# Performance work log

Measured on AMD Instinct MI355X. Metric: run time of the kernel, lower is better.

Reference implementation:

```python
import jax, jax.numpy as jnp
import numpy as np

B, T, D, H = 4, 2048, 1024, 16
HS = D // H  # 64
SCALE = float(HS) ** (-5)  # faithful to source: head_size ** (-5), NOT -0.5
EPS = 1e-5


def layer_norm(x, g, b):
    m = jnp.mean(x, axis=-1, keepdims=True)
    v = jnp.mean(jnp.square(x - m), axis=-1, keepdims=True)
    return (x - m) * jax.lax.rsqrt(v + EPS) * g + b


def setup_inputs() -> dict:
    key = jax.random.key(0)
    ks = jax.random.split(key, 8)
    s = 0.02
    return {
        "x": jax.random.normal(ks[0], (B, T, D), dtype=jnp.float32),
        "Wk": jax.random.normal(ks[1], (H, D, HS), dtype=jnp.float32) * s,  # shared by q (source bug: q = self.key(x))
        "Wv": jax.random.normal(ks[2], (H, D, HS), dtype=jnp.float32) * s,
        "Wo": jax.random.normal(ks[3], (H * HS, D), dtype=jnp.float32) * s,
        "bo": jnp.zeros((D,), dtype=jnp.float32),
        "g1": jnp.ones((D,), dtype=jnp.float32),
        "b1": jnp.zeros((D,), dtype=jnp.float32),
        "Wf1": jax.random.normal(ks[4], (D, D), dtype=jnp.float32) * s,
        "bf1": jnp.zeros((D,), dtype=jnp.float32),
        "Wf2": jax.random.normal(ks[5], (D, D), dtype=jnp.float32) * s,
        "bf2": jnp.zeros((D,), dtype=jnp.float32),
        "g2": jnp.ones((D,), dtype=jnp.float32),
        "b2": jnp.zeros((D,), dtype=jnp.float32),
    }


def reference(x, Wk, Wv, Wo, bo, g1, b1, Wf1, bf1, Wf2, bf2, g2, b2):
    # per-head projections; source uses key weights for BOTH q and k, so q == k
    k = jnp.einsum('btd,hds->bhts', x, Wk)           # [B,H,T,HS]
    v = jnp.einsum('btd,hds->bhts', x, Wv)           # [B,H,T,HS]
    wei = jnp.einsum('bhts,bhus->bhtu', k, k) * SCALE  # q==k; [B,H,T,T]
    causal = jnp.tril(jnp.ones((T, T), dtype=bool))
    wei = jnp.where(causal, wei, -jnp.inf)
    wei = jax.nn.softmax(wei, axis=-1)
    attn = jnp.einsum('bhtu,bhus->bhts', wei, v)     # [B,H,T,HS]
    cat = attn.transpose(0, 2, 1, 3).reshape(B, T, H * HS)  # concat heads
    attn_out = cat @ Wo + bo                         # output projection
    norm = layer_norm(attn_out + x, g1, b1)
    ff = jax.nn.relu(norm @ Wf1 + bf1) @ Wf2 + bf2
    return layer_norm(ff + norm + x, g2, b2)
```

## Files before the change

kernel.cpp:

```cpp
#include <hip/hip_runtime.h>

typedef unsigned short u16;
typedef __attribute__((ext_vector_type(8))) short short8;
typedef __attribute__((ext_vector_type(4))) float f32x4;

constexpr int Bn = 4, Tn = 2048, Dn = 1024, Hn = 16, HSn = 64;
constexpr long BT = (long)Bn * Tn;
#define NSEG 64
#define SEG (Tn / NSEG)

__device__ __forceinline__ u16 f2bf(float f) {
    union { float f; unsigned u; } x; x.f = f;
    unsigned r = x.u + 0x7FFFu + ((x.u >> 16) & 1u);
    return (u16)(r >> 16);
}
__device__ __forceinline__ float bf2f(unsigned bits16) {
    union { unsigned u; float f; } x; x.u = bits16 << 16;
    return x.f;
}

__device__ __forceinline__ void async_load16(const u16* g, u16* lds) {
    __builtin_amdgcn_global_load_lds(
        (const __attribute__((address_space(1))) unsigned*)g,
        (__attribute__((address_space(3))) unsigned*)lds, 16, 0, 0);
}

__global__ __launch_bounds__(256) void prep_kernel(
    const float* __restrict__ x, const float* __restrict__ Wv,
    const float* __restrict__ Wo, const float* __restrict__ Wf1,
    const float* __restrict__ Wf2,
    u16* __restrict__ xb, u16* __restrict__ WvC,
    u16* __restrict__ WoT, u16* __restrict__ Wf1T, u16* __restrict__ Wf2T)
{
    __shared__ float tile[32][33];
    const int blk = blockIdx.x;
    if (blk < 8192) {
        long i = (long)blk * 256 + threadIdx.x;
        float4 v = ((const float4*)x)[i];
        unsigned lo = (unsigned)f2bf(v.x) | ((unsigned)f2bf(v.y) << 16);
        unsigned hi = (unsigned)f2bf(v.z) | ((unsigned)f2bf(v.w) << 16);
        ((uint2*)xb)[i] = make_uint2(lo, hi);
    } else if (blk < 12288) {
        long i = (long)(blk - 8192) * 256 + threadIdx.x;
        int d = (int)(i >> 10), c = (int)(i & 1023);
        int h = c >> 6, s = c & 63;
        WvC[i] = f2bf(Wv[((long)h * Dn + d) * HSn + s]);
    } else {
        int idx = blk - 12288;
        int z = idx >> 10, rem = idx & 1023;
        const float* in = z == 0 ? Wo : (z == 1 ? Wf1 : Wf2);
        u16* out        = z == 0 ? WoT : (z == 1 ? Wf1T : Wf2T);
        int k0 = (rem & 31) * 32, n0 = (rem >> 5) * 32;
        int tx = threadIdx.x & 31, ty = threadIdx.x >> 5;
        #pragma unroll
        for (int r = 0; r < 4; r++)
            tile[ty + r * 8][tx] = in[(long)(k0 + ty + r * 8) * Dn + n0 + tx];
        __syncthreads();
        #pragma unroll
        for (int r = 0; r < 4; r++)
            out[(long)(n0 + ty + r * 8) * Dn + k0 + tx] = f2bf(tile[tx][ty + r * 8]);
    }
}

__device__ __forceinline__ void stageA256(const u16* __restrict__ Ag, u16* la,
                                          int r, int wv, int ln, int row0,
                                          int K, int kt) {
    int Ib = r * 512 + wv * 64;
    int I = Ib + ln;
    int m = I >> 3, pc = I & 7, c = pc ^ (m & 7);
    async_load16(&Ag[(long)(row0 + m) * K + kt * 64 + c * 8], &la[Ib * 8]);
}
__device__ __forceinline__ void stageB256(const u16* __restrict__ Bg, u16* lb,
                                          int r, int wv, int ln, int n0,
                                          int K, int kt) {
    int Ib = r * 512 + wv * 64;
    int I = Ib + ln;
    int m = I >> 3, pc = I & 7, c = pc ^ (m & 7);
    async_load16(&Bg[(long)(n0 + m) * K + kt * 64 + c * 8], &lb[Ib * 8]);
}
__device__ __forceinline__ short8 ldfrag(const u16* ls, int row, int lc) {
    return *(const short8*)&ls[(row * 8 + (lc ^ (row & 7))) * 8];
}

__global__ __launch_bounds__(512) void mfma_gemm256(
    const u16* __restrict__ A,
    const u16* __restrict__ BTm,
    u16* __restrict__ Cb,
    const float* __restrict__ bias, int relu, int K, int N,
    float* __restrict__ segs_out)
{
    __shared__ __attribute__((aligned(16))) u16 As[3][256 * 64];
    __shared__ __attribute__((aligned(16))) u16 Bs[3][128 * 64];

    const int t = threadIdx.x;
    const int wv = t >> 6, ln = t & 63;
    const int lane15 = ln & 15, qq = ln >> 4;
    const int wr = wv >> 2, wc = wv & 3;
    const int row0 = blockIdx.x * 256, n0 = blockIdx.y * 128;
    const int NT = K >> 6;

    f32x4 acc[8][2];
    #pragma unroll
    for (int i = 0; i < 8; i++)
        #pragma unroll
        for (int j = 0; j < 2; j++)
            acc[i][j] = (f32x4){0.f, 0.f, 0.f, 0.f};

    u16 *A0 = &As[0][0], *A1 = &As[1][0], *A2 = &As[2][0];
    u16 *B0 = &Bs[0][0], *B1 = &Bs[1][0], *B2 = &Bs[2][0];

    #pragma unroll
    for (int r = 0; r < 4; r++) stageA256(A, A0, r, wv, ln, row0, K, 0);
    #pragma unroll
    for (int r = 0; r < 2; r++) stageB256(BTm, B0, r, wv, ln, n0, K, 0);
    #pragma unroll
    for (int r = 0; r < 4; r++) stageA256(A, A1, r, wv, ln, row0, K, 1);
    #pragma unroll
    for (int r = 0; r < 2; r++) stageB256(BTm, B1, r, wv, ln, n0, K, 1);
    asm volatile("s_waitcnt vmcnt(6)" ::: "memory");
    __builtin_amdgcn_s_barrier();

    for (int kt = 0; kt < NT; kt++) {
        const bool st = (kt + 2 < NT);
        short8 bq[2][2];
        #pragma unroll
        for (int ph = 0; ph < 4; ph++) {
            short8 af[2][2];
            #pragma unroll
            for (int ii = 0; ii < 2; ii++) {
                int ar = wr * 128 + (ph * 2 + ii) * 16 + lane15;
                af[ii][0] = ldfrag(A0, ar, qq);
                af[ii][1] = ldfrag(A0, ar, 4 + qq);
            }
            if (ph == 0) {
                #pragma unroll
                for (int ng = 0; ng < 2; ng++) {
                    int br = wc * 32 + ng * 16 + lane15;
                    bq[ng][0] = ldfrag(B0, br, qq);
                    bq[ng][1] = ldfrag(B0, br, 4 + qq);
                }
                if (st) {
                    stageA256(A, A2, 0, wv, ln, row0, K, kt + 2);
                    stageA256(A, A2, 1, wv, ln, row0, K, kt + 2);
                }
            } else if (ph == 1) {
                if (st) {
                    stageA256(A, A2, 2, wv, ln, row0, K, kt + 2);
                    stageA256(A, A2, 3, wv, ln, row0, K, kt + 2);
                }
            } else if (ph == 2) {
                if (st) {
                    stageB256(BTm, B2, 0, wv, ln, n0, K, kt + 2);
                    stageB256(BTm, B2, 1, wv, ln, n0, K, kt + 2);
                }
            }
            __builtin_amdgcn_s_barrier();
            __builtin_amdgcn_s_setprio(1);
            #pragma unroll
            for (int kk = 0; kk < 2; kk++)
                #pragma unroll
                for (int ii = 0; ii < 2; ii++)
                    #pragma unroll
                    for (int ng = 0; ng < 2; ng++)
                        acc[ph * 2 + ii][ng] = __builtin_amdgcn_mfma_f32_16x16x32_bf16(
                            af[ii][kk], bq[ng][kk], acc[ph * 2 + ii][ng], 0, 0, 0);
            __builtin_amdgcn_s_setprio(0);
            if (ph < 3) {
                __builtin_amdgcn_s_barrier();
            } else if (kt < NT - 1) {
                if (st) asm volatile("s_waitcnt vmcnt(6)" ::: "memory");
                else    asm volatile("s_waitcnt vmcnt(0)" ::: "memory");
                __builtin_amdgcn_s_barrier();
            }
        }
        u16* ta = A0; A0 = A1; A1 = A2; A2 = ta;
        u16* tb = B0; B0 = B1; B1 = B2; B2 = tb;
    }

    if (segs_out) {
        int segbase = blockIdx.x * 8 + wr * 4;
        #pragma unroll
        for (int s = 0; s < 4; s++) {
            #pragma unroll
            for (int ng = 0; ng < 2; ng++) {
                float sum = 0.f;
                #pragma unroll
                for (int r = 0; r < 4; r++)
                    sum += acc[2 * s][ng][r] + acc[2 * s + 1][ng][r];
                sum += __shfl_xor(sum, 16);
                sum += __shfl_xor(sum, 32);
                if (qq == 0) {
                    int col = n0 + wc * 32 + ng * 16 + lane15;
                    segs_out[(long)(segbase + s) * N + col] = sum;
                }
            }
        }
    }

    #pragma unroll
    for (int ng = 0; ng < 2; ng++) {
        int col = n0 + wc * 32 + ng * 16 + lane15;
        float bv = bias ? bias[col] : 0.f;
        #pragma unroll
        for (int i = 0; i < 8; i++) {
            #pragma unroll
            for (int r = 0; r < 4; r++) {
                long row = row0 + wr * 128 + i * 16 + qq * 4 + r;
                float v = acc[i][ng][r] + bv;
                if (relu) v = fmaxf(v, 0.f);
                Cb[row * N + col] = f2bf(v);
            }
        }
    }
}

__global__ __launch_bounds__(256) void mfma_gemm64(
    const u16* __restrict__ A, const u16* __restrict__ BT,
    u16* __restrict__ Cb, int K, int N)
{
    __shared__ __attribute__((aligned(16))) u16 As[64 * 64];
    __shared__ __attribute__((aligned(16))) u16 Bs[64 * 64];

    const int t = threadIdx.x;
    const int wv = t >> 6, ln = t & 63;
    const int lane15 = ln & 15, q = ln >> 4;
    const int row0 = blockIdx.x * 64, n0 = blockIdx.y * 64;
    const int mq = (wv >> 1) * 32, nq = (wv & 1) * 32;

    f32x4 acc[2][2];
    #pragma unroll
    for (int i = 0; i < 2; i++)
        #pragma unroll
        for (int j = 0; j < 2; j++)
            acc[i][j] = (f32x4){0.f, 0.f, 0.f, 0.f};

    for (int k0 = 0; k0 < K; k0 += 64) {
        #pragma unroll
        for (int jj = 0; jj < 2; jj++) {
            int Ibase = wv * 128 + jj * 64;
            int I = Ibase + ln;
            int m = I >> 3, pc = I & 7, c = pc ^ (m & 7);
            async_load16(&A[(long)(row0 + m) * K + k0 + c * 8], &As[Ibase * 8]);
        }
        #pragma unroll
        for (int jj = 0; jj < 2; jj++) {
            int Ibase = wv * 128 + jj * 64;
            int I = Ibase + ln;
            int m = I >> 3, pc = I & 7, c = pc ^ (m & 7);
            async_load16(&BT[(long)(n0 + m) * K + k0 + c * 8], &Bs[Ibase * 8]);
        }
        __syncthreads();

        #pragma unroll
        for (int kk = 0; kk < 2; kk++) {
            short8 af[2], bfr[2];
            #pragma unroll
            for (int i = 0; i < 2; i++) {
                int mr = mq + i * 16 + lane15;
                int ca = (kk * 4 + q) ^ (mr & 7);
                af[i] = *(const short8*)&As[(mr * 8 + ca) * 8];
                int nr = nq + i * 16 + lane15;
                int cb = (kk * 4 + q) ^ (nr & 7);
                bfr[i] = *(const short8*)&Bs[(nr * 8 + cb) * 8];
            }
            #pragma unroll
            for (int i = 0; i < 2; i++)
                #pragma unroll
                for (int j = 0; j < 2; j++)
                    acc[i][j] = __builtin_amdgcn_mfma_f32_16x16x32_bf16(
                        af[i], bfr[j], acc[i][j], 0, 0, 0);
        }
        __syncthreads();
    }

    #pragma unroll
    for (int j = 0; j < 2; j++) {
        int col = n0 + nq + j * 16 + lane15;
        #pragma unroll
        for (int i = 0; i < 2; i++)
            #pragma unroll
            for (int r = 0; r < 4; r++) {
                long row = row0 + mq + i * 16 + q * 4 + r;
                Cb[row * N + col] = f2bf(acc[i][j][r]);
            }
    }
}

__global__ __launch_bounds__(256) void scanln_kernel(
    const u16* __restrict__ y, const float* __restrict__ segs,
    const float* __restrict__ bo, const u16* __restrict__ xb,
    const float* __restrict__ g1, const float* __restrict__ b1,
    u16* __restrict__ nb)
{
    __shared__ float zs[16 * 1024];

    const int b = blockIdx.x, sg = blockIdx.y;
    const int t = threadIdx.x;
    const int lane = t & 63, w = t >> 6;

    float r0 = 0.f, r1 = 0.f, r2 = 0.f, r3 = 0.f;
    for (int s = 0; s < sg; s++) {
        float4 sv = ((const float4*)&segs[((long)(b * NSEG + s)) * Dn])[t];
        r0 += sv.x; r1 += sv.y; r2 += sv.z; r3 += sv.w;
    }
    const float4 bv = ((const float4*)bo)[t];

    float gv[16], be[16];
    #pragma unroll
    for (int j = 0; j < 4; j++) {
        *(float4*)&gv[j * 4] = *(const float4*)(g1 + j * 256 + lane * 4);
        *(float4*)&be[j * 4] = *(const float4*)(b1 + j * 256 + lane * 4);
    }

    const long rowu = ((long)b * Tn + (long)sg * SEG) * (Dn / 2);
    const unsigned* yu = (const unsigned*)y  + rowu;
    const unsigned* xu = (const unsigned*)xb + rowu;
    unsigned*       nu = (unsigned*)nb       + rowu;
    const int tb = sg * SEG;

    #pragma unroll
    for (int half = 0; half < 2; half++) {
        if (half) __syncthreads();
        for (int tt = 0; tt < 16; tt++) {
            int rowl = half * 16 + tt;
            uint2 uy = *(const uint2*)(yu + (long)rowl * 512 + 2 * t);
            r0 += bf2f(uy.x & 0xFFFFu); r1 += bf2f(uy.x >> 16);
            r2 += bf2f(uy.y & 0xFFFFu); r3 += bf2f(uy.y >> 16);
            uint2 ux = *(const uint2*)(xu + (long)rowl * 512 + 2 * t);
            float inv = 1.0f / (float)(tb + rowl + 1);
            float4 z4;
            z4.x = r0 * inv + bv.x + bf2f(ux.x & 0xFFFFu);
            z4.y = r1 * inv + bv.y + bf2f(ux.x >> 16);
            z4.z = r2 * inv + bv.z + bf2f(ux.y & 0xFFFFu);
            z4.w = r3 * inv + bv.w + bf2f(ux.y >> 16);
            *(float4*)&zs[tt * 1024 + 4 * t] = z4;
        }
        __syncthreads();
        #pragma unroll
        for (int k = 0; k < 4; k++) {
            int zrow = w * 4 + k;
            float f[16];
            #pragma unroll
            for (int j = 0; j < 4; j++)
                *(float4*)&f[j * 4] = *(const float4*)&zs[zrow * 1024 + j * 256 + lane * 4];
            float s = 0.f, ss = 0.f;
            #pragma unroll
            for (int i = 0; i < 16; i++) { s += f[i]; ss += f[i] * f[i]; }
            #pragma unroll
            for (int o = 1; o <= 32; o <<= 1) {
                s += __shfl_xor(s, o); ss += __shfl_xor(ss, o);
            }
            float mean = s * (1.0f / Dn);
            float var = ss * (1.0f / Dn) - mean * mean;
            float is = rsqrtf(var + 1e-5f);
            unsigned* op = nu + (long)(half * 16 + zrow) * 512;
            #pragma unroll
            for (int j = 0; j < 4; j++) {
                float e0 = (f[j * 4 + 0] - mean) * is * gv[j * 4 + 0] + be[j * 4 + 0];
                float e1 = (f[j * 4 + 1] - mean) * is * gv[j * 4 + 1] + be[j * 4 + 1];
                float e2 = (f[j * 4 + 2] - mean) * is * gv[j * 4 + 2] + be[j * 4 + 2];
                float e3 = (f[j * 4 + 3] - mean) * is * gv[j * 4 + 3] + be[j * 4 + 3];
                uint2 pk;
                pk.x = (unsigned)f2bf(e0) | ((unsigned)f2bf(e1) << 16);
                pk.y = (unsigned)f2bf(e2) | ((unsigned)f2bf(e3) << 16);
                *(uint2*)(op + j * 128 + 2 * lane) = pk;
            }
        }
    }
}

__global__ __launch_bounds__(256) void ln_kernel(
    const u16* __restrict__ a, const u16* __restrict__ b,
    const u16* __restrict__ c,
    const float* __restrict__ g, const float* __restrict__ beta,
    float* __restrict__ outf)
{
    const long base2 = (long)blockIdx.x * (Dn / 2);
    const int t = threadIdx.x;
    uint2 ua = ((const uint2*)((const unsigned*)a + base2))[t];
    float vx = bf2f(ua.x & 0xFFFFu), vy = bf2f(ua.x >> 16);
    float vz = bf2f(ua.y & 0xFFFFu), vw = bf2f(ua.y >> 16);
    uint2 ub = ((const uint2*)((const unsigned*)b + base2))[t];
    vx += bf2f(ub.x & 0xFFFFu); vy += bf2f(ub.x >> 16);
    vz += bf2f(ub.y & 0xFFFFu); vw += bf2f(ub.y >> 16);
    uint2 uc = ((const uint2*)((const unsigned*)c + base2))[t];
    vx += bf2f(uc.x & 0xFFFFu); vy += bf2f(uc.x >> 16);
    vz += bf2f(uc.y & 0xFFFFu); vw += bf2f(uc.y >> 16);

    __shared__ float sred[8];
    const int lane = t & 63, w = t >> 6;

    float s = vx + vy + vz + vw;
    #pragma unroll
    for (int o = 32; o > 0; o >>= 1) s += __shfl_down(s, o);
    if (lane == 0) sred[w] = s;
    __syncthreads();
    float mean = (sred[0] + sred[1] + sred[2] + sred[3]) * (1.0f / Dn);

    float dx = vx - mean, dy = vy - mean, dz = vz - mean, dw = vw - mean;
    float qq = dx * dx + dy * dy + dz * dz + dw * dw;
    #pragma unroll
    for (int o = 32; o > 0; o >>= 1) qq += __shfl_down(qq, o);
    if (lane == 0) sred[4 + w] = qq;
    __syncthreads();
    float var = (sred[4] + sred[5] + sred[6] + sred[7]) * (1.0f / Dn);
    float inv = rsqrtf(var + 1e-5f);

    float4 gg = ((const float4*)g)[t];
    float4 bb = ((const float4*)beta)[t];
    ((float4*)outf)[(long)blockIdx.x * 256 + t] = make_float4(
        dx * inv * gg.x + bb.x, dy * inv * gg.y + bb.y,
        dz * inv * gg.z + bb.z, dw * inv * gg.w + bb.w);
}

extern "C" void kernel_launch(void* const* d_in, const int* in_sizes, int n_in,
                              void* d_out, int out_size, void* d_ws, size_t ws_size,
                              hipStream_t stream) {
    const float* x   = (const float*)d_in[0];
    const float* Wv  = (const float*)d_in[2];
    const float* Wo  = (const float*)d_in[3];
    const float* bo  = (const float*)d_in[4];
    const float* g1  = (const float*)d_in[5];
    const float* b1  = (const float*)d_in[6];
    const float* Wf1 = (const float*)d_in[7];
    const float* bf1 = (const float*)d_in[8];
    const float* Wf2 = (const float*)d_in[9];
    const float* bf2 = (const float*)d_in[10];
    const float* g2  = (const float*)d_in[11];
    const float* b2  = (const float*)d_in[12];
    float* out = (float*)d_out;

    float* segs = (float*)d_ws;
    u16* xb   = (u16*)(segs + (long)Bn * NSEG * Dn);
    u16* yb   = xb + BT * Dn;
    u16* nb   = yb + BT * Dn;
    u16* fb   = nb + BT * Dn;
    u16* WoT  = fb + BT * Dn;
    u16* Wf1T = WoT + (long)Dn * Dn;
    u16* Wf2T = Wf1T + (long)Dn * Dn;
    u16* WvC  = Wf2T + (long)Dn * Dn;
    u16* WvoT = WvC + (long)Dn * Dn;

    dim3 blk(256);

    prep_kernel<<<dim3(15360), blk, 0, stream>>>(
        x, Wv, Wo, Wf1, Wf2, xb, WvC, WoT, Wf1T, Wf2T);

    mfma_gemm64<<<dim3(16, 16), blk, 0, stream>>>(WoT, WvC, WvoT, Dn, Dn);

    dim3 ggrid(BT / 256, Dn / 128);
    dim3 gblk(512);
    mfma_gemm256<<<ggrid, gblk, 0, stream>>>(
        xb, WvoT, yb, nullptr, 0, Dn, Dn, segs);
    scanln_kernel<<<dim3(Bn, NSEG), blk, 0, stream>>>(
        yb, segs, bo, xb, g1, b1, nb);
    mfma_gemm256<<<ggrid, gblk, 0, stream>>>(
        nb, Wf1T, fb, bf1, 1, Dn, Dn, nullptr);
    mfma_gemm256<<<ggrid, gblk, 0, stream>>>(
        fb, Wf2T, yb, bf2, 0, Dn, Dn, nullptr);
    ln_kernel<<<dim3((unsigned)BT), blk, 0, stream>>>(
        yb, nb, xb, g2, b2, out);
}
```

Before: 139.7 us.

## Switch 256x128 GEMM to 32x32x16 MFMA with 4x2 wave layout

Replaces the 16x16x32 bf16 MFMA tiles with 32x32x16 MFMA and remaps the 8 waves from a 2x4 grid to a 4x2 grid. Each wave now computes 64x64 instead of 128x32. The four-phase k-loop becomes two phases, with the async staging of the next tiles redistributed across them. The larger MFMA shape is meant to cut LDS fragment reads per FLOP and the number of barriers. The segment-sum and epilogue indexing are rewritten for the 32x32 accumulator layout, which risks index errors. Fewer barriers also means less overlap between global loads and compute.

```diff
diff --git a/kernel.cpp b/kernel.cpp
--- a/kernel.cpp
+++ b/kernel.cpp
@@ -3,6 +3,7 @@
 typedef unsigned short u16;
 typedef __attribute__((ext_vector_type(8))) short short8;
 typedef __attribute__((ext_vector_type(4))) float f32x4;
+typedef __attribute__((ext_vector_type(16))) float f32x16;
 
 constexpr int Bn = 4, Tn = 2048, Dn = 1024, Hn = 16, HSn = 64;
 constexpr long BT = (long)Bn * Tn;
@@ -94,17 +95,18 @@
 
     const int t = threadIdx.x;
     const int wv = t >> 6, ln = t & 63;
-    const int lane15 = ln & 15, qq = ln >> 4;
-    const int wr = wv >> 2, wc = wv & 3;
+    const int l31 = ln & 31, hf = ln >> 5;
+    const int wr = wv >> 1, wc = wv & 1;
     const int row0 = blockIdx.x * 256, n0 = blockIdx.y * 128;
     const int NT = K >> 6;
 
-    f32x4 acc[8][2];
-    #pragma unroll
-    for (int i = 0; i < 8; i++)
+    f32x16 acc[2][2];
+    #pragma unroll
+    for (int i = 0; i < 2; i++)
         #pragma unroll
         for (int j = 0; j < 2; j++)
-            acc[i][j] = (f32x4){0.f, 0.f, 0.f, 0.f};
+            #pragma unroll
+            for (int r = 0; r < 16; r++) acc[i][j][r] = 0.f;
 
     u16 *A0 = &As[0][0], *A1 = &As[1][0], *A2 = &As[2][0];
     u16 *B0 = &Bs[0][0], *B1 = &Bs[1][0], *B2 = &Bs[2][0];
@@ -122,96 +124,100 @@
 
     for (int kt = 0; kt < NT; kt++) {
         const bool st = (kt + 2 < NT);
-        short8 bq[2][2];
-        #pragma unroll
-        for (int ph = 0; ph < 4; ph++) {
-            short8 af[2][2];
-            #pragma unroll
-            for (int ii = 0; ii < 2; ii++) {
-                int ar = wr * 128 + (ph * 2 + ii) * 16 + lane15;
-                af[ii][0] = ldfrag(A0, ar, qq);
-                af[ii][1] = ldfrag(A0, ar, 4 + qq);
-            }
-            if (ph == 0) {
+        short8 af[2][2], bfq[2][2];
+        #pragma unroll
+        for (int mf = 0; mf < 2; mf++)
+            #pragma unroll
+            for (int ks = 0; ks < 2; ks++)
+                af[mf][ks] = ldfrag(A0, wr * 64 + mf * 32 + l31, 2 * ks + hf);
+        #pragma unroll
+        for (int nf = 0; nf < 2; nf++)
+            #pragma unroll
+            for (int ks = 0; ks < 2; ks++)
+                bfq[nf][ks] = ldfrag(B0, wc * 64 + nf * 32 + l31, 2 * ks + hf);
+        if (st) {
+            stageA256(A, A2, 0, wv, ln, row0, K, kt + 2);
+            stageA256(A, A2, 1, wv, ln, row0, K, kt + 2);
+            stageA256(A, A2, 2, wv, ln, row0, K, kt + 2);
+        }
+        __builtin_amdgcn_s_barrier();
+        __builtin_amdgcn_s_setprio(1);
+        #pragma unroll
+        for (int ks = 0; ks < 2; ks++)
+            #pragma unroll
+            for (int mf = 0; mf < 2; mf++)
                 #pragma unroll
-                for (int ng = 0; ng < 2; ng++) {
-                    int br = wc * 32 + ng * 16 + lane15;
-                    bq[ng][0] = ldfrag(B0, br, qq);
-                    bq[ng][1] = ldfrag(B0, br, 4 + qq);
-                }
-                if (st) {
-                    stageA256(A, A2, 0, wv, ln, row0, K, kt + 2);
-                    stageA256(A, A2, 1, wv, ln, row0, K, kt + 2);
-                }
-            } else if (ph == 1) {
-                if (st) {
-                    stageA256(A, A2, 2, wv, ln, row0, K, kt + 2);
-                    stageA256(A, A2, 3, wv, ln, row0, K, kt + 2);
-                }
-            } else if (ph == 2) {
-                if (st) {
-                    stageB256(BTm, B2, 0, wv, ln, n0, K, kt + 2);
-                    stageB256(BTm, B2, 1, wv, ln, n0, K, kt + 2);
-                }
-            }
+                for (int nf = 0; nf < 2; nf++)
+                    acc[mf][nf] = __builtin_amdgcn_mfma_f32_32x32x16_bf16(
+                        af[mf][ks], bfq[nf][ks], acc[mf][nf], 0, 0, 0);
+        __builtin_amdgcn_s_setprio(0);
+        __builtin_amdgcn_s_barrier();
+        #pragma unroll
+        for (int mf = 0; mf < 2; mf++)
+            #pragma unroll
+            for (int ks = 0; ks < 2; ks++)
+                af[mf][ks] = ldfrag(A0, wr * 64 + mf * 32 + l31, 4 + 2 * ks + hf);
+        #pragma unroll
+        for (int nf = 0; nf < 2; nf++)
+            #pragma unroll
+            for (int ks = 0; ks < 2; ks++)
+                bfq[nf][ks] = ldfrag(B0, wc * 64 + nf * 32 + l31, 4 + 2 * ks + hf);
+        if (st) {
+            stageA256(A, A2, 3, wv, ln, row0, K, kt + 2);
+            stageB256(BTm, B2, 0, wv, ln, n0, K, kt + 2);
+            stageB256(BTm, B2, 1, wv, ln, n0, K, kt + 2);
+        }
+        __builtin_amdgcn_s_barrier();
+        __builtin_amdgcn_s_setprio(1);
+        #pragma unroll
+        for (int ks = 0; ks < 2; ks++)
+            #pragma unroll
+            for (int mf = 0; mf < 2; mf++)
+                #pragma unroll
+                for (int nf = 0; nf < 2; nf++)
+                    acc[mf][nf] = __builtin_amdgcn_mfma_f32_32x32x16_bf16(
+                        af[mf][ks], bfq[nf][ks], acc[mf][nf], 0, 0, 0);
+        __builtin_amdgcn_s_setprio(0);
+        if (kt < NT - 1) {
+            if (st) asm volatile("s_waitcnt vmcnt(6)" ::: "memory");
+            else    asm volatile("s_waitcnt vmcnt(0)" ::: "memory");
             __builtin_amdgcn_s_barrier();
-            __builtin_amdgcn_s_setprio(1);
-            #pragma unroll
-            for (int kk = 0; kk < 2; kk++)
-                #pragma unroll
-                for (int ii = 0; ii < 2; ii++)
-                    #pragma unroll
-                    for (int ng = 0; ng < 2; ng++)
-                        acc[ph * 2 + ii][ng] = __builtin_amdgcn_mfma_f32_16x16x32_bf16(
-                            af[ii][kk], bq[ng][kk], acc[ph * 2 + ii][ng], 0, 0, 0);
-            __builtin_amdgcn_s_setprio(0);
-            if (ph < 3) {
-                __builtin_amdgcn_s_barrier();
-            } else if (kt < NT - 1) {
-                if (st) asm volatile("s_waitcnt vmcnt(6)" ::: "memory");
-                else    asm volatile("s_waitcnt vmcnt(0)" ::: "memory");
-                __builtin_amdgcn_s_barrier();
-            }
         }
         u16* ta = A0; A0 = A1; A1 = A2; A2 = ta;
         u16* tb = B0; B0 = B1; B1 = B2; B2 = tb;
     }
 
     if (segs_out) {
-        int segbase = blockIdx.x * 8 + wr * 4;
-        #pragma unroll
-        for (int s = 0; s < 4; s++) {
-            #pragma unroll
-            for (int ng = 0; ng < 2; ng++) {
-                float sum = 0.f;
+        int segbase = blockIdx.x * 8 + wr * 2;
+        #pragma unroll
+        for (int mf = 0; mf < 2; mf++)
+            #pragma unroll
+            for (int nf = 0; nf < 2; nf++) {
+                float s = 0.f;
                 #pragma unroll
-                for (int r = 0; r < 4; r++)
-                    sum += acc[2 * s][ng][r] + acc[2 * s + 1][ng][r];
-                sum += __shfl_xor(sum, 16);
-                sum += __shfl_xor(sum, 32);
-                if (qq == 0) {
-                    int col = n0 + wc * 32 + ng * 16 + lane15;
-                    segs_out[(long)(segbase + s) * N + col] = sum;
+                for (int r = 0; r < 16; r++) s += acc[mf][nf][r];
+                s += __shfl_xor(s, 32);
+                if (hf == 0) {
+                    int col = n0 + wc * 64 + nf * 32 + l31;
+                    segs_out[(long)(segbase + mf) * N + col] = s;
                 }
             }
-        }
-    }
-
-    #pragma unroll
-    for (int ng = 0; ng < 2; ng++) {
-        int col = n0 + wc * 32 + ng * 16 + lane15;
-        float bv = bias ? bias[col] : 0.f;
-        #pragma unroll
-        for (int i = 0; i < 8; i++) {
-            #pragma unroll
-            for (int r = 0; r < 4; r++) {
-                long row = row0 + wr * 128 + i * 16 + qq * 4 + r;
-                float v = acc[i][ng][r] + bv;
+    }
+
+    #pragma unroll
+    for (int mf = 0; mf < 2; mf++)
+        #pragma unroll
+        for (int nf = 0; nf < 2; nf++) {
+            int col = n0 + wc * 64 + nf * 32 + l31;
+            float bv = bias ? bias[col] : 0.f;
+            #pragma unroll
+            for (int r = 0; r < 16; r++) {
+                long row = row0 + wr * 64 + mf * 32 + (r & 3) + 8 * (r >> 2) + 4 * hf;
+                float v = acc[mf][nf][r] + bv;
                 if (relu) v = fmaxf(v, 0.f);
                 Cb[row * N + col] = f2bf(v);
             }
         }
-    }
 }
 
 __global__ __launch_bounds__(256) void mfma_gemm64(
```

New measurement: 143.8 us. 1.03x slower.

## Fuse final FFN GEMM with residual add and second layernorm

Applied to the files above, without the earlier changes.

Replaces the last GEMM plus separate layernorm kernel with one kernel where each block computes 32 full rows of the output. Bias, residuals and the row-wise layernorm are applied from the accumulators via shuffle and LDS reductions, avoiding the bf16 intermediate write and re-read plus a launch. The GEMM loads operands directly from global memory without LDS tiling and only launches 256 blocks, which may reduce GEMM efficiency. Variance now uses the E[z^2]-mean^2 form.

```diff
diff --git a/kernel.cpp b/kernel.cpp
--- a/kernel.cpp
+++ b/kernel.cpp
@@ -3,6 +3,7 @@
 typedef unsigned short u16;
 typedef __attribute__((ext_vector_type(8))) short short8;
 typedef __attribute__((ext_vector_type(4))) float f32x4;
+typedef __attribute__((ext_vector_type(16))) float f32x16;
 
 constexpr int Bn = 4, Tn = 2048, Dn = 1024, Hn = 16, HSn = 64;
 constexpr long BT = (long)Bn * Tn;
@@ -369,48 +370,110 @@
     }
 }
 
-__global__ __launch_bounds__(256) void ln_kernel(
-    const u16* __restrict__ a, const u16* __restrict__ b,
-    const u16* __restrict__ c,
-    const float* __restrict__ g, const float* __restrict__ beta,
-    float* __restrict__ outf)
+__global__ __launch_bounds__(512) void gemmln_kernel(
+    const u16* __restrict__ A,
+    const u16* __restrict__ BTm,
+    const float* __restrict__ bias,
+    const u16* __restrict__ nb, const u16* __restrict__ xb,
+    const float* __restrict__ g2, const float* __restrict__ b2,
+    float* __restrict__ out)
 {
-    const long base2 = (long)blockIdx.x * (Dn / 2);
+    __shared__ float sred[32][8];
+    __shared__ float qred[32][8];
+
     const int t = threadIdx.x;
-    uint2 ua = ((const uint2*)((const unsigned*)a + base2))[t];
-    float vx = bf2f(ua.x & 0xFFFFu), vy = bf2f(ua.x >> 16);
-    float vz = bf2f(ua.y & 0xFFFFu), vw = bf2f(ua.y >> 16);
-    uint2 ub = ((const uint2*)((const unsigned*)b + base2))[t];
-    vx += bf2f(ub.x & 0xFFFFu); vy += bf2f(ub.x >> 16);
-    vz += bf2f(ub.y & 0xFFFFu); vw += bf2f(ub.y >> 16);
-    uint2 uc = ((const uint2*)((const unsigned*)c + base2))[t];
-    vx += bf2f(uc.x & 0xFFFFu); vy += bf2f(uc.x >> 16);
-    vz += bf2f(uc.y & 0xFFFFu); vw += bf2f(uc.y >> 16);
-
-    __shared__ float sred[8];
-    const int lane = t & 63, w = t >> 6;
-
-    float s = vx + vy + vz + vw;
-    #pragma unroll
-    for (int o = 32; o > 0; o >>= 1) s += __shfl_down(s, o);
-    if (lane == 0) sred[w] = s;
+    const int wv = t >> 6, ln = t & 63;
+    const int l31 = ln & 31, hf = ln >> 5;
+    const int row0 = blockIdx.x * 32;
+    const int c0 = wv * 128;
+
+    f32x16 acc[4];
+    #pragma unroll
+    for (int nf = 0; nf < 4; nf++)
+        #pragma unroll
+        for (int r = 0; r < 16; r++) acc[nf][r] = 0.f;
+
+    const u16* Ap = A + (long)(row0 + l31) * 1024 + hf * 8;
+    const u16* Bp = BTm + (long)(c0 + l31) * 1024 + hf * 8;
+
+    #pragma unroll 2
+    for (int kt = 0; kt < 16; kt++) {
+        short8 af[4], bq[4][4];
+        #pragma unroll
+        for (int ks = 0; ks < 4; ks++)
+            af[ks] = *(const short8*)(Ap + kt * 64 + ks * 16);
+        #pragma unroll
+        for (int nf = 0; nf < 4; nf++)
+            #pragma unroll
+            for (int ks = 0; ks < 4; ks++)
+                bq[nf][ks] = *(const short8*)(Bp + (long)nf * 32 * 1024 + kt * 64 + ks * 16);
+        #pragma unroll
+        for (int ks = 0; ks < 4; ks++)
+            #pragma unroll
+            for (int nf = 0; nf < 4; nf++)
+                acc[nf] = __builtin_amdgcn_mfma_f32_32x32x16_bf16(
+                    af[ks], bq[nf][ks], acc[nf], 0, 0, 0);
+    }
+
+    #pragma unroll
+    for (int nf = 0; nf < 4; nf++) {
+        int col = c0 + nf * 32 + l31;
+        float bv = bias[col];
+        #pragma unroll
+        for (int r = 0; r < 16; r++) {
+            int row = (r & 3) + 8 * (r >> 2) + 4 * hf;
+            long g = (long)(row0 + row) * 1024 + col;
+            acc[nf][r] += bv + bf2f(nb[g]) + bf2f(xb[g]);
+        }
+    }
+
+    float ps[16], pq[16];
+    #pragma unroll
+    for (int r = 0; r < 16; r++) {
+        float s = 0.f, q = 0.f;
+        #pragma unroll
+        for (int nf = 0; nf < 4; nf++) {
+            float z = acc[nf][r];
+            s += z; q += z * z;
+        }
+        #pragma unroll
+        for (int o = 1; o <= 16; o <<= 1) {
+            s += __shfl_xor(s, o); q += __shfl_xor(q, o);
+        }
+        ps[r] = s; pq[r] = q;
+    }
+    if (l31 == 0) {
+        #pragma unroll
+        for (int r = 0; r < 16; r++) {
+            int row = (r & 3) + 8 * (r >> 2) + 4 * hf;
+            sred[row][wv] = ps[r];
+            qred[row][wv] = pq[r];
+        }
+    }
     __syncthreads();
-    float mean = (sred[0] + sred[1] + sred[2] + sred[3]) * (1.0f / Dn);
-
-    float dx = vx - mean, dy = vy - mean, dz = vz - mean, dw = vw - mean;
-    float qq = dx * dx + dy * dy + dz * dz + dw * dw;
-    #pragma unroll
-    for (int o = 32; o > 0; o >>= 1) qq += __shfl_down(qq, o);
-    if (lane == 0) sred[4 + w] = qq;
-    __syncthreads();
-    float var = (sred[4] + sred[5] + sred[6] + sred[7]) * (1.0f / Dn);
-    float inv = rsqrtf(var + 1e-5f);
-
-    float4 gg = ((const float4*)g)[t];
-    float4 bb = ((const float4*)beta)[t];
-    ((float4*)outf)[(long)blockIdx.x * 256 + t] = make_float4(
-        dx * inv * gg.x + bb.x, dy * inv * gg.y + bb.y,
-        dz * inv * gg.z + bb.z, dw * inv * gg.w + bb.w);
+
+    float gg[4], bb[4];
+    #pragma unroll
+    for (int nf = 0; nf < 4; nf++) {
+        int col = c0 + nf * 32 + l31;
+        gg[nf] = g2[col]; bb[nf] = b2[col];
+    }
+    #pragma unroll
+    for (int r = 0; r < 16; r++) {
+        int row = (r & 3) + 8 * (r >> 2) + 4 * hf;
+        float s = 0.f, q = 0.f;
+        #pragma unroll
+        for (int w2 = 0; w2 < 8; w2++) { s += sred[row][w2]; q += qred[row][w2]; }
+        float mean = s * (1.0f / Dn);
+        float var = q * (1.0f / Dn) - mean * mean;
+        float inv = rsqrtf(var + 1e-5f);
+        #pragma unroll
+        for (int nf = 0; nf < 4; nf++) {
+            int col = c0 + nf * 32 + l31;
+            out[(long)(row0 + row) * 1024 + col] =
+                (acc[nf][r] - mean) * inv * gg[nf] + bb[nf];
+        }
+    }
 }
 
 extern "C" void kernel_launch(void* const* d_in, const int* in_sizes, int n_in,
@@ -456,8 +519,6 @@
         yb, segs, bo, xb, g1, b1, nb);
     mfma_gemm256<<<ggrid, gblk, 0, stream>>>(
         nb, Wf1T, fb, bf1, 1, Dn, Dn, nullptr);
-    mfma_gemm256<<<ggrid, gblk, 0, stream>>>(
-        fb, Wf2T, yb, bf2, 0, Dn, Dn, nullptr);
-    ln_kernel<<<dim3((unsigned)BT), blk, 0, stream>>>(
-        yb, nb, xb, g2, b2, out);
-}
+    gemmln_kernel<<<dim3(256), gblk, 0, stream>>>(
+        fb, Wf2T, bf2, nb, xb, g2, b2, out);
+}
```

Measured after the change: 196.8 us. 40.8% more time.
